# Performance work log

Hardware: AMD Instinct MI355X
Metric: run time of the kernel (lower is better)

## Reference

```python
import jax, jax.numpy as jnp
import numpy as np

B, T, D, H, W = 2, 16, 64, 64, 64
MAX_GROWTH = 0.0  # max_growth_rate init kwarg

def _ln(x, g, b):
    m = x.mean(-1, keepdims=True)
    v = x.var(-1, keepdims=True)
    return (x - m) * jax.lax.rsqrt(v + 1e-5) * g + b

def _pscan(A, X):
    # linear recurrence h_t = A_t*h_{t-1} + X_t via Blelchlo-style associative scan over axis 1
    def comb(l, r):
        a1, x1 = l
        a2, x2 = r
        return a1 * a2, a2 * x1 + x2
    return jax.lax.associative_scan(comb, (A, X), axis=1)[1]

def setup_inputs() -> dict:
    key = jax.random.key(0)
    ks = jax.random.split(key, 20)
    n = lambda k, s, sc=1.0: jax.random.normal(k, s, dtype=jnp.float32) * sc
    inp = dict(
        x_re=n(ks[0], (B, T, D, H, W)), x_im=n(ks[1], (B, T, D, H, W)),
        h_re=n(ks[2], (B * H * W, 1, D)), h_im=n(ks[3], (B * H * W, 1, D)),
        flux_re=n(ks[4], (B, D)), flux_im=n(ks[5], (B, D)),
        dt_seq=0.01 + 0.1 * jax.random.uniform(ks[6], (B, T), dtype=jnp.float32),
        g_s=jnp.ones(2 * D, jnp.float32), b_s=jnp.zeros(2 * D, jnp.float32),
        Wc=n(ks[7], (3, 3, 2 * D, 2 * D), 1.0 / np.sqrt(9 * 2 * D)), bc=jnp.zeros(2 * D, jnp.float32),
        g_t=jnp.ones(2 * D, jnp.float32), b_t=jnp.zeros(2 * D, jnp.float32),
        E_re=n(ks[8], (D, D), 1.0 / np.sqrt(D)), E_im=n(ks[9], (D, D), 1.0 / np.sqrt(D)),
        Dec_re=n(ks[10], (D, D), 1.0 / np.sqrt(D)), Dec_im=n(ks[11], (D, D), 1.0 / np.sqrt(D)),
        lam_flux_raw=jnp.zeros(D, jnp.float32),
        Wsrc_re=n(ks[12], (D, D), 1.0 / np.sqrt(D)), Wsrc_im=n(ks[13], (D, D), 1.0 / np.sqrt(D)),
        w_gate=n(ks[14], (D,)), b_gate=jnp.zeros(D, jnp.float32),
        lam_re_raw=jnp.ones(D, jnp.float32), lam_im=n(ks[15], (D,)),
        W1=n(ks[16], (2 * D, 8 * D), 1.0 / np.sqrt(2 * D)), b1=jnp.zeros(8 * D, jnp.float32),
        W2=n(ks[17], (8 * D, 2 * D), 1.0 / np.sqrt(8 * D)), b2=jnp.zeros(2 * D, jnp.float32),
    )
    return inp

def _forward(x_re, x_im, h_re, h_im, flux_re, flux_im, dt_seq, g_s, b_s, Wc, bc, g_t, b_t,
             E_re, E_im, Dec_re, Dec_im, lam_flux_raw, Wsrc_re, Wsrc_im, w_gate, b_gate,
             lam_re_raw, lam_im, W1, b1, W2, b2):
    # channel-last complex field (B,T,H,W,D)
    x = jnp.moveaxis(x_re, 2, -1) + 1j * jnp.moveaxis(x_im, 2, -1)
    # --- spatial residual branch: LN -> Clifford(= real 2D conv on [re;im] channels) ---
    xr = jnp.concatenate([x.real, x.imag], -1)  # (B,T,H,W,2D)
    xn = _ln(xr, g_s, b_s).reshape(B * T, H, W, 2 * D)
    xs = jax.lax.conv_general_dilated(xn, Wc, (1, 1), 'SAME',
                                      dimension_numbers=('NHWC', 'HWIO', 'NHWC')) + bc
    xs = xs.reshape(B, T, H, W, 2 * D)
    x = x + (xs[..., :D] + 1j * xs[..., D:])
    # --- eigen-basis encode ---
    x_eig = jnp.einsum('bthwd,de->bthwe', x, E_re + 1j * E_im)
    x_mean = x_eig.mean((2, 3))  # (B,T,D)
    # --- flux tracker scan ---
    lam_f = jax.nn.softplus(lam_flux_raw)
    A_flux = jnp.exp(-lam_f * dt_seq[..., None])  # (B,T,D) real decay
    flux = _pscan(A_flux.astype(x_mean.dtype), x_mean * dt_seq[..., None])
    flux = flux + (flux_re + 1j * flux_im)[:, None, :] * jnp.cumprod(A_flux, axis=1)
    source = jnp.einsum('btd,de->bte', flux, Wsrc_re + 1j * Wsrc_im)
    gate = jax.nn.sigmoid(flux.real * w_gate + b_gate)  # real gate in [0,1]
    flux_out = flux[:, -1]
    ge = gate[:, :, None, None, :]
    forcing = x_eig * ge + source[:, :, None, None, :] * (1.0 - ge)
    # --- temporal propagator (exact exponential integrator) ---
    lam = (MAX_GROWTH - jax.nn.softplus(lam_re_raw)) + 1j * lam_im  # Re(lam) <= max_growth_rate
    op_decay = jnp.exp(lam * dt_seq[..., None])            # (B,T,D)
    op_forcing = (op_decay - 1.0) / lam
    u = forcing * op_forcing[:, :, None, None, :]          # (B,T,H,W,D)
    h_prev = (h_re + 1j * h_im).reshape(B, H, W, D)
    u = u.at[:, 0].add(h_prev * op_decay[:, 0][:, None, None, :])
    A_full = jnp.broadcast_to(op_decay[:, :, None, None, :], u.shape)
    u_out = _pscan(A_full, u)                              # (B,T,H,W,D)
    h_out = u_out[:, -1].reshape(B * H * W, 1, D)
    # --- decode + temporal LN/FFN residual ---
    decoded = jnp.einsum('bthwd,de->bthwe', u_out, Dec_re + 1j * Dec_im)
    dn = _ln(jnp.concatenate([decoded.real, decoded.imag], -1), g_t, b_t)
    h1 = jax.nn.gelu(jnp.einsum('bthwc,cf->bthwf', dn, W1) + b1)
    d2 = jnp.einsum('bthwf,fc->bthwc', h1, W2) + b2
    delta = d2[..., :D] + 1j * d2[..., D:]
    z = x + decoded + delta
    return z, h_out, flux_out

def reference(x_re, x_im, h_re, h_im, flux_re, flux_im, dt_seq, g_s, b_s, Wc, bc, g_t, b_t,
              E_re, E_im, Dec_re, Dec_im, lam_flux_raw, Wsrc_re, Wsrc_im, w_gate, b_gate,
              lam_re_raw, lam_im, W1, b1, W2, b2):
    z, h_out, flux_out = _forward(x_re, x_im, h_re, h_im, flux_re, flux_im, dt_seq, g_s, b_s,
                                  Wc, bc, g_t, b_t, E_re, E_im, Dec_re, Dec_im, lam_flux_raw,
                                  Wsrc_re, Wsrc_im, w_gate, b_gate, lam_re_raw, lam_im,
                                  W1, b1, W2, b2)
    # complex outputs returned as real/imag stacked on last axis
    return (jnp.stack([z.real, z.imag], -1),
            jnp.stack([h_out.real, h_out.imag], -1),
            jnp.stack([flux_out.real, flux_out.imag], -1))
```

## Files before the change

### kernel.cpp

```cpp
#include <hip/hip_runtime.h>
#include <hip/hip_bf16.h>


typedef __hip_bfloat16 bf16;
typedef __attribute__((ext_vector_type(8))) short bhalf8;
typedef __attribute__((ext_vector_type(4))) float floatx4;

#define DEV __device__ __forceinline__

DEV float b2f(const bf16 x) { return __bfloat162float(x); }
DEV bf16  f2b(float x)      { return __float2bfloat16(x); }
DEV unsigned short f2bu(float x) { bf16 h = f2b(x); return *(unsigned short*)&h; }
DEV float bu2f(unsigned short u) { unsigned int t = ((unsigned int)u) << 16; return *(float*)&t; }
DEV float softplusf(float x){ return x > 20.f ? x : log1pf(expf(x)); }
DEV float geluf(float x) {
    float v = x * fmaf(x * x, 0.10294324f, 2.30220819f);
    float e = __builtin_amdgcn_exp2f(-v);
    return x * __builtin_amdgcn_rcpf(1.f + e);
}

static constexpr int B_ = 2, T_ = 16, D_ = 64, HW = 4096;
static constexpr int NPIX = B_ * T_ * HW;
static constexpr long long N1 = (long long)NPIX * 128;

static constexpr long long BUFA  = 0;
static constexpr long long XUBF  = N1;
static constexpr long long DECBF = N1 + N1 / 2;
static constexpr long long XNBF  = 2 * N1;
static constexpr long long XCBF  = 2 * N1 + N1 / 2;
static constexpr long long XMEAN = 3 * N1;
static constexpr long long TABS  = XMEAN + 4096;
static constexpr long long FLAGO = TABS + 14336;
static constexpr long long WCP   = FLAGO + 64;
static constexpr long long W1P   = WCP + 73728;
static constexpr long long W2P   = W1P + 32768;
static constexpr long long WEP   = W2P + 32768;
static constexpr long long WDP   = WEP + 8192;

static constexpr long long ZOUT = 0;
static constexpr long long HOUT = 16777216;
static constexpr long long FOUT = 17825792;

DEV float ld(const void* p, long long i, bool bf) {
    if (bf) return b2f(((const bf16*)p)[i]);
    return ((const float*)p)[i];
}

__global__ void k_detect(const unsigned short* __restrict__ x, float* __restrict__ ws) {
    int lane = threadIdx.x;
    int cnt = 0;
    for (int i = lane; i < 256; i += 64) {
        int e = (x[i] >> 7) & 0xFF;
        cnt += (e >= 100 && e <= 140) ? 1 : 0;
    }
    for (int m = 1; m < 64; m <<= 1) cnt += __shfl_xor(cnt, m, 64);
    if (lane == 0) ws[FLAGO] = (cnt >= 224) ? 1.f : 0.f;
}

__global__ void k_convert(const void* Wc, const void* W1, const void* W2,
                          const void* Er, const void* Ei, const void* Dr, const void* Di,
                          float* ws) {
    bool bf = ws[FLAGO] != 0.f;
    int i = blockIdx.x * 256 + threadIdx.x;
    unsigned short* wcp = (unsigned short*)(ws + WCP);
    unsigned short* w1p = (unsigned short*)(ws + W1P);
    unsigned short* w2p = (unsigned short*)(ws + W2P);
    unsigned short* wep = (unsigned short*)(ws + WEP);
    unsigned short* wdp = (unsigned short*)(ws + WDP);
    if (i < 147456) {
        int j = i & 7, lane = (i >> 3) & 63, nt = (i >> 9) & 7, kc = (i >> 12) & 3, tap = i >> 14;
        int ic = kc * 32 + ((lane >> 4) << 3) + j, oc = nt * 16 + (lane & 15);
        wcp[i] = f2bu(ld(Wc, tap * 16384 + ic * 128 + oc, bf)); return;
    } i -= 147456;
    if (i < 65536) {
        int j = i & 7, lane = (i >> 3) & 63, nt = (i >> 9) & 31, kc = i >> 14;
        int ic = kc * 32 + ((lane >> 4) << 3) + j, oc = nt * 16 + (lane & 15);
        w1p[i] = f2bu(ld(W1, ic * 512 + oc, bf)); return;
    } i -= 65536;
    if (i < 65536) {
        int j = i & 7, lane = (i >> 3) & 63, nt = (i >> 9) & 7, kc = i >> 12;
        int ic = kc * 32 + ((lane >> 4) << 3) + j, oc = nt * 16 + (lane & 15);
        w2p[i] = f2bu(ld(W2, ic * 128 + oc, bf)); return;
    } i -= 65536;
    if (i < 16384) {
        int j = i & 7, lane = (i >> 3) & 63, nt = (i >> 9) & 7, kc = i >> 12;
        int k = kc * 32 + ((lane >> 4) << 3) + j, n = nt * 16 + (lane & 15);
        float v;
        if (k < 64) v = (n < 64) ? ld(Er, k * 64 + n, bf) : ld(Ei, k * 64 + (n - 64), bf);
        else        v = (n < 64) ? -ld(Ei, (k - 64) * 64 + n, bf) : ld(Er, (k - 64) * 64 + (n - 64), bf);
        wep[i] = f2bu(v); return;
    } i -= 16384;
    if (i < 16384) {
        int j = i & 7, lane = (i >> 3) & 63, nt = (i >> 9) & 7, kc = i >> 12;
        int k = kc * 32 + ((lane >> 4) << 3) + j, n = nt * 16 + (lane & 15);
        float v;
        if (k < 64) v = (n < 64) ? ld(Dr, k * 64 + n, bf) : ld(Di, k * 64 + (n - 64), bf);
        else        v = (n < 64) ? -ld(Di, (k - 64) * 64 + n, bf) : ld(Dr, (k - 64) * 64 + (n - 64), bf);
        wdp[i] = f2bu(v); return;
    }
}

__global__ __launch_bounds__(256) void kA_ln(const void* __restrict__ xre,
                                             const void* __restrict__ xim,
                                             const void* __restrict__ gs,
                                             const void* __restrict__ bs,
                                             float* __restrict__ ws) {
    __shared__ unsigned short sr[64][72] __attribute__((aligned(16)));
    __shared__ unsigned short si[64][72] __attribute__((aligned(16)));
    __shared__ float red[2][4][64];
    __shared__ float mv[64], rv[64], gb[256];
    bool bf = ws[FLAGO] != 0.f;
    int blk = blockIdx.x;
    int bt = blk >> 6;
    int px0 = (blk & 63) * 64;
    int tid = threadIdx.x;
    gb[tid] = (tid < 128) ? ld(gs, tid, bf) : ld(bs, tid - 128, bf);
    if (bf) {
        const unsigned short* xr16 = (const unsigned short*)xre;
        const unsigned short* xi16 = (const unsigned short*)xim;
        for (int l = tid; l < 1024; l += 256) {
            int a = l >> 9, dd = (l >> 3) & 63, ck = l & 7;
            long long src = (long long)bt * 262144 + (long long)dd * 4096 + px0 + ck * 8;
            bhalf8 v = *(const bhalf8*)&(a ? xi16 : xr16)[src];
            *(bhalf8*)&(a ? si : sr)[dd][ck * 8] = v;
        }
    } else {
        for (int l = tid; l < 8192; l += 256) {
            int a = l >> 12, dd = (l >> 6) & 63, px = l & 63;
            float v = ((const float*)(a ? xim : xre))[(long long)bt * 262144 + (long long)dd * 4096 + px0 + px];
            (a ? si : sr)[dd][px] = f2bu(v);
        }
    }
    __syncthreads();
    int px = tid & 63, part = tid >> 6;
    float s = 0.f, ss = 0.f;
    for (int d = part * 16; d < part * 16 + 16; d++) {
        float r = bu2f(sr[d][px]), q = bu2f(si[d][px]);
        s += r + q; ss += r * r + q * q;
    }
    red[0][part][px] = s; red[1][part][px] = ss;
    __syncthreads();
    if (tid < 64) {
        float S  = red[0][0][tid] + red[0][1][tid] + red[0][2][tid] + red[0][3][tid];
        float SS = red[1][0][tid] + red[1][1][tid] + red[1][2][tid] + red[1][3][tid];
        float m = S * (1.f / 128.f);
        mv[tid] = m;
        rv[tid] = rsqrtf(SS * (1.f / 128.f) - m * m + 1e-5f);
    }
    __syncthreads();
    unsigned short* xcb = (unsigned short*)(ws + XCBF);
    unsigned short* xnb = (unsigned short*)(ws + XNBF);
    long long pbase = ((long long)bt * 4096 + px0) * 128;
    for (int l = tid; l < 8192; l += 256) {
        int p2 = l >> 7, ch = l & 127, d = ch & 63;
        unsigned short raw = (ch < 64 ? sr : si)[d][p2];
        float v = bu2f(raw);
        xcb[pbase + p2 * 128 + ch] = raw;
        xnb[pbase + p2 * 128 + ch] = f2bu((v - mv[p2]) * rv[p2] * gb[ch] + gb[128 + ch]);
    }
}

__global__ __launch_bounds__(256) void kB_conv(const void* __restrict__ bc,
                                               float* __restrict__ ws) {
    __shared__ unsigned short xt[3][64][136] __attribute__((aligned(16)));
    bool bf = ws[FLAGO] != 0.f;
    int blk = blockIdx.x, bt = blk >> 6, h = blk & 63;
    int tid = threadIdx.x, lane = tid & 63, wv = tid >> 6;
    int m16 = lane & 15, quad = lane >> 4;
    const unsigned short* xnb = (const unsigned short*)(ws + XNBF);
    const unsigned short* wcp = (const unsigned short*)(ws + WCP);
    bhalf8 zero8 = {0, 0, 0, 0, 0, 0, 0, 0};
    for (int l = tid; l < 3072; l += 256) {
        int r = l >> 10, rem = l & 1023, col = rem >> 4, ck = rem & 15;
        int hr = h - 1 + r;
        bhalf8 v = zero8;
        if (hr >= 0 && hr < 64)
            v = *(const bhalf8*)&xnb[(((long long)bt * 4096 + hr * 64 + col) << 7) + ck * 8];
        *(bhalf8*)&xt[r][col][ck * 8] = v;
    }
    __syncthreads();
    floatx4 acc[4][2];
    #pragma unroll
    for (int mt = 0; mt < 4; mt++)
        #pragma unroll
        for (int nt = 0; nt < 2; nt++)
            acc[mt][nt] = (floatx4){0.f, 0.f, 0.f, 0.f};
    for (int tap = 0; tap < 9; tap++) {
        int dy = tap / 3, dx = tap - dy * 3;
        #pragma unroll
        for (int kc = 0; kc < 4; kc++) {
            bhalf8 bfr[2];
            #pragma unroll
            for (int nt = 0; nt < 2; nt++)
                bfr[nt] = *(const bhalf8*)&wcp[((((tap * 4 + kc) * 8) + (wv * 2 + nt)) * 64 + lane) * 8];
            #pragma unroll
            for (int mt = 0; mt < 4; mt++) {
                int col = mt * 16 + m16 + dx - 1;
                bhalf8 af = zero8;
                if (col >= 0 && col < 64)
                    af = *(const bhalf8*)&xt[dy][col][kc * 32 + quad * 8];
                acc[mt][0] = __builtin_amdgcn_mfma_f32_16x16x32_bf16(af, bfr[0], acc[mt][0], 0, 0, 0);
                acc[mt][1] = __builtin_amdgcn_mfma_f32_16x16x32_bf16(af, bfr[1], acc[mt][1], 0, 0, 0);
            }
        }
    }
    __syncthreads();
    unsigned short (*At)[136] = (unsigned short(*)[136])&xt[0][0][0];
    const unsigned short* xcb = (const unsigned short*)(ws + XCBF);
    unsigned short* xub = (unsigned short*)(ws + XUBF);
    #pragma unroll
    for (int nt = 0; nt < 2; nt++) {
        int n = wv * 32 + nt * 16 + m16;
        float bcv = ld(bc, n, bf);
        #pragma unroll
        for (int mt = 0; mt < 4; mt++)
            #pragma unroll
            for (int r = 0; r < 4; r++) {
                int m = mt * 16 + quad * 4 + r;
                long long p = (long long)bt * 4096 + h * 64 + m;
                unsigned short u = f2bu(acc[mt][nt][r] + bu2f(xcb[p * 128 + n]) + bcv);
                xub[p * 128 + n] = u;
                At[m][n] = u;
            }
    }
    __syncthreads();
    const unsigned short* wep = (const unsigned short*)(ws + WEP);
    long long px0 = (long long)blk * 64;
    floatx4 acce[4][2];
    #pragma unroll
    for (int mt = 0; mt < 4; mt++)
        #pragma unroll
        for (int nt = 0; nt < 2; nt++)
            acce[mt][nt] = (floatx4){0.f, 0.f, 0.f, 0.f};
    #pragma unroll
    for (int kc = 0; kc < 4; kc++) {
        bhalf8 bfr[2];
        #pragma unroll
        for (int nt = 0; nt < 2; nt++)
            bfr[nt] = *(const bhalf8*)&wep[(((kc * 8) + wv * 2 + nt) * 64 + lane) * 8];
        #pragma unroll
        for (int mt = 0; mt < 4; mt++) {
            bhalf8 af = *(const bhalf8*)&At[mt * 16 + m16][kc * 32 + quad * 8];
            acce[mt][0] = __builtin_amdgcn_mfma_f32_16x16x32_bf16(af, bfr[0], acce[mt][0], 0, 0, 0);
            acce[mt][1] = __builtin_amdgcn_mfma_f32_16x16x32_bf16(af, bfr[1], acce[mt][1], 0, 0, 0);
        }
    }
    unsigned short* xeb = (unsigned short*)(ws + BUFA);
    #pragma unroll
    for (int nt = 0; nt < 2; nt++) {
        int n = wv * 32 + nt * 16 + m16;
        float part = 0.f;
        #pragma unroll
        for (int mt = 0; mt < 4; mt++)
            #pragma unroll
            for (int r = 0; r < 4; r++) {
                int m = mt * 16 + quad * 4 + r;
                xeb[(px0 + m) * 128 + n] = f2bu(acce[mt][nt][r]);
                part += acce[mt][nt][r];
            }
        part += __shfl_xor(part, 16, 64);
        part += __shfl_xor(part, 32, 64);
        if (quad == 0) atomicAdd(ws + XMEAN + bt * 128 + n, part);
    }
}

__global__ __launch_bounds__(256) void kD_flux(const void* __restrict__ fxr, const void* __restrict__ fxi,
                                               const void* __restrict__ dtseq, const void* __restrict__ lamflux,
                                               const void* __restrict__ Wsr, const void* __restrict__ Wsi,
                                               const void* __restrict__ wgate, const void* __restrict__ bgate,
                                               const void* __restrict__ lamreraw, const void* __restrict__ lamim,
                                               float* __restrict__ ws, void* __restrict__ outv) {
    bool bfo = ws[FLAGO] != 0.f;
    int b = blockIdx.x;
    int tid = threadIdx.x;
    int d = tid & 63, g = tid >> 6;
    __shared__ float fr[64], fi[64], psr[4][64], psi[4][64];
    float lam_f = softplusf(ld(lamflux, d, bfo));
    float lre = -softplusf(ld(lamreraw, d, bfo));
    float lim = ld(lamim, d, bfo);
    float cr = 0.f, ci = 0.f;
    if (g == 0) { cr = ld(fxr, b * 64 + d, bfo); ci = ld(fxi, b * 64 + d, bfo); }
    float* tabs = ws + TABS;
    const float* xmean = ws + XMEAN;
    for (int t = 0; t < 16; t++) {
        float dt = ld(dtseq, b * 16 + t, bfo);
        int idx = b * 1024 + t * 64 + d;
        if (g == 0) {
            float A = expf(-lam_f * dt);
            float xr = xmean[(b * 16 + t) * 128 + d]      * (1.f / 4096.f) * dt;
            float xq = xmean[(b * 16 + t) * 128 + 64 + d] * (1.f / 4096.f) * dt;
            cr = A * cr + xr; ci = A * ci + xq;
            fr[d] = cr; fi[d] = ci;
        }
        __syncthreads();
        {
            float pr = 0.f, pi = 0.f;
            #pragma unroll
            for (int k = 0; k < 16; k++) {
                int d2 = g * 16 + k;
                float wr = ld(Wsr, d2 * 64 + d, bfo), wi = ld(Wsi, d2 * 64 + d, bfo);
                pr += fr[d2] * wr - fi[d2] * wi;
                pi += fr[d2] * wi + fi[d2] * wr;
            }
            psr[g][d] = pr; psi[g][d] = pi;
        }
        if (g == 1) {
            float od  = expf(lre * dt);
            float odr = od * cosf(lim * dt);
            float odi = od * sinf(lim * dt);
            tabs[3 * 2048 + idx] = odr; tabs[4 * 2048 + idx] = odi;
            float den = lre * lre + lim * lim;
            float tr = odr - 1.f;
            tabs[5 * 2048 + idx] = (tr * lre + odi * lim) / den;
            tabs[6 * 2048 + idx] = (odi * lre - tr * lim) / den;
        }
        __syncthreads();
        if (g == 0) {
            float sr = psr[0][d] + psr[1][d] + psr[2][d] + psr[3][d];
            float si2 = psi[0][d] + psi[1][d] + psi[2][d] + psi[3][d];
            tabs[1 * 2048 + idx] = sr; tabs[2 * 2048 + idx] = si2;
            tabs[0 * 2048 + idx] = 1.f / (1.f + expf(-(cr * ld(wgate, d, bfo) + ld(bgate, d, bfo))));
            if (t == 15) {
                if (bfo) {
                    bf16* ob = (bf16*)outv;
                    ob[FOUT + (b * 64 + d) * 2]     = f2b(cr);
                    ob[FOUT + (b * 64 + d) * 2 + 1] = f2b(ci);
                } else {
                    float* of = (float*)outv;
                    of[FOUT + (b * 64 + d) * 2]     = cr;
                    of[FOUT + (b * 64 + d) * 2 + 1] = ci;
                }
            }
        }
    }
}

__global__ __launch_bounds__(256) void kE_scan(const void* __restrict__ hre,
                                               const void* __restrict__ him,
                                               float* __restrict__ ws, void* __restrict__ outv) {
    __shared__ float tab[7][16][64];
    bool bfo = ws[FLAGO] != 0.f;
    int tid = threadIdx.x;
    long long G = (long long)blockIdx.x * 256 + tid;
    int d0 = (int)(G & 31) * 2;
    int pixg = (int)(G >> 5);
    int pix = pixg & 4095;
    int b = pixg >> 12;
    const float* tabs = ws + TABS;
    for (int l = tid; l < 7 * 1024; l += 256) {
        int a = l >> 10, idx = l & 1023;
        ((float*)tab)[l] = tabs[a * 2048 + b * 1024 + idx];
    }
    __syncthreads();
    long long hidx = ((long long)b * 4096 + pix) * 64 + d0;
    float cr0, ci0, cr1, ci1;
    if (bfo) {
        unsigned int r2 = *(const unsigned int*)&((const unsigned short*)hre)[hidx];
        unsigned int i2 = *(const unsigned int*)&((const unsigned short*)him)[hidx];
        cr0 = bu2f((unsigned short)(r2 & 0xffff)); cr1 = bu2f((unsigned short)(r2 >> 16));
        ci0 = bu2f((unsigned short)(i2 & 0xffff)); ci1 = bu2f((unsigned short)(i2 >> 16));
    } else {
        float2 r2 = *(const float2*)((const float*)hre + hidx);
        float2 i2 = *(const float2*)((const float*)him + hidx);
        cr0 = r2.x; cr1 = r2.y; ci0 = i2.x; ci1 = i2.y;
    }
    const unsigned short* xe = (const unsigned short*)(ws + BUFA);
    unsigned short* ub = (unsigned short*)(ws + XCBF);
    for (int t = 0; t < 16; t++) {
        long long base = ((long long)((b * 16 + t) * 4096 + pix)) * 128 + d0;
        unsigned int xr2 = *(const unsigned int*)&xe[base];
        unsigned int xi2 = *(const unsigned int*)&xe[base + 64];
        float2 gt2  = *(const float2*)&tab[0][t][d0];
        float2 sr2  = *(const float2*)&tab[1][t][d0];
        float2 si2  = *(const float2*)&tab[2][t][d0];
        float2 odr2 = *(const float2*)&tab[3][t][d0];
        float2 odi2 = *(const float2*)&tab[4][t][d0];
        float2 ofr2 = *(const float2*)&tab[5][t][d0];
        float2 ofi2 = *(const float2*)&tab[6][t][d0];
        {
            float xr = bu2f((unsigned short)(xr2 & 0xffff));
            float xi = bu2f((unsigned short)(xi2 & 0xffff));
            float fre = xr * gt2.x + sr2.x * (1.f - gt2.x);
            float fim = xi * gt2.x + si2.x * (1.f - gt2.x);
            float ure = fre * ofr2.x - fim * ofi2.x;
            float uim = fre * ofi2.x + fim * ofr2.x;
            float n0 = odr2.x * cr0 - odi2.x * ci0 + ure;
            float n1 = odr2.x * ci0 + odi2.x * cr0 + uim;
            cr0 = n0; ci0 = n1;
        }
        {
            float xr = bu2f((unsigned short)(xr2 >> 16));
            float xi = bu2f((unsigned short)(xi2 >> 16));
            float fre = xr * gt2.y + sr2.y * (1.f - gt2.y);
            float fim = xi * gt2.y + si2.y * (1.f - gt2.y);
            float ure = fre * ofr2.y - fim * ofi2.y;
            float uim = fre * ofi2.y + fim * ofr2.y;
            float n0 = odr2.y * cr1 - odi2.y * ci1 + ure;
            float n1 = odr2.y * ci1 + odi2.y * cr1 + uim;
            cr1 = n0; ci1 = n1;
        }
        *(unsigned int*)&ub[base]      = (unsigned int)f2bu(cr0) | ((unsigned int)f2bu(cr1) << 16);
        *(unsigned int*)&ub[base + 64] = (unsigned int)f2bu(ci0) | ((unsigned int)f2bu(ci1) << 16);
    }
    if (bfo) {
        uint2 hv;
        hv.x = (unsigned int)f2bu(cr0) | ((unsigned int)f2bu(ci0) << 16);
        hv.y = (unsigned int)f2bu(cr1) | ((unsigned int)f2bu(ci1) << 16);
        *(uint2*)((unsigned short*)outv + HOUT + 2 * hidx) = hv;
    } else {
        float4 hv; hv.x = cr0; hv.y = ci0; hv.z = cr1; hv.w = ci1;
        *(float4*)((float*)outv + HOUT + 2 * hidx) = hv;
    }
}

__global__ __launch_bounds__(256, 4) void kMLP(const void* __restrict__ gt_,
                                               const void* __restrict__ bt_,
                                               const void* __restrict__ b1v,
                                               const void* __restrict__ b2v,
                                               float* __restrict__ ws, void* __restrict__ outv) {
    __shared__ unsigned char POOL[16384] __attribute__((aligned(16)));
    __shared__ unsigned short Dt[32][136] __attribute__((aligned(16)));
    __shared__ unsigned short A1[32][136] __attribute__((aligned(16)));
    __shared__ float gbt[256];
    __shared__ float gb2[128];
    __shared__ float psS[4][32], psQ[4][32];
    __shared__ float mvv[32], rvv[32];
    unsigned short (*UA)[136] = (unsigned short(*)[136])POOL;
    unsigned short (*h1f)[2][64][8] = (unsigned short(*)[2][64][8])POOL;
    bool bf = ws[FLAGO] != 0.f;
    long long px0 = (long long)blockIdx.x * 32;
    int tid = threadIdx.x, lane = tid & 63, wv = tid >> 6;
    int m16 = lane & 15, quad = lane >> 4;
    gbt[tid] = (tid < 128) ? ld(gt_, tid, bf) : ld(bt_, tid - 128, bf);
    if (tid < 128) gb2[tid] = ld(b2v, tid, bf);
    const unsigned short* uo = (const unsigned short*)(ws + XCBF);
    for (int l = tid; l < 512; l += 256) {
        int p2 = l >> 4, ck = l & 15;
        *(bhalf8*)&UA[p2][ck * 8] = *(const bhalf8*)&uo[(px0 + p2) * 128 + ck * 8];
    }
    __syncthreads();
    const unsigned short* wdp = (const unsigned short*)(ws + WDP);
    floatx4 accd[2][2];
    #pragma unroll
    for (int mt = 0; mt < 2; mt++)
        #pragma unroll
        for (int nt = 0; nt < 2; nt++)
            accd[mt][nt] = (floatx4){0.f, 0.f, 0.f, 0.f};
    #pragma unroll
    for (int kc = 0; kc < 4; kc++) {
        bhalf8 bfr0 = *(const bhalf8*)&wdp[(((kc * 8) + wv * 2 + 0) * 64 + lane) * 8];
        bhalf8 bfr1 = *(const bhalf8*)&wdp[(((kc * 8) + wv * 2 + 1) * 64 + lane) * 8];
        bhalf8 af0 = *(const bhalf8*)&UA[m16][kc * 32 + quad * 8];
        bhalf8 af1 = *(const bhalf8*)&UA[16 + m16][kc * 32 + quad * 8];
        accd[0][0] = __builtin_amdgcn_mfma_f32_16x16x32_bf16(af0, bfr0, accd[0][0], 0, 0, 0);
        accd[0][1] = __builtin_amdgcn_mfma_f32_16x16x32_bf16(af0, bfr1, accd[0][1], 0, 0, 0);
        accd[1][0] = __builtin_amdgcn_mfma_f32_16x16x32_bf16(af1, bfr0, accd[1][0], 0, 0, 0);
        accd[1][1] = __builtin_amdgcn_mfma_f32_16x16x32_bf16(af1, bfr1, accd[1][1], 0, 0, 0);
    }
    #pragma unroll
    for (int mt = 0; mt < 2; mt++)
        #pragma unroll
        for (int r = 0; r < 4; r++) {
            int mrow = mt * 16 + quad * 4 + r;
            float a0 = accd[mt][0][r], a1 = accd[mt][1][r];
            Dt[mrow][wv * 32 + m16]      = f2bu(a0);
            Dt[mrow][wv * 32 + 16 + m16] = f2bu(a1);
            float s = a0 + a1, q = a0 * a0 + a1 * a1;
            #pragma unroll
            for (int msk = 1; msk <= 8; msk <<= 1) {
                s += __shfl_xor(s, msk, 64);
                q += __shfl_xor(q, msk, 64);
            }
            if (m16 == 0) { psS[wv][mrow] = s; psQ[wv][mrow] = q; }
        }
    __syncthreads();
    if (tid < 32) {
        float S = psS[0][tid] + psS[1][tid] + psS[2][tid] + psS[3][tid];
        float Q = psQ[0][tid] + psQ[1][tid] + psQ[2][tid] + psQ[3][tid];
        float m = S * (1.f / 128.f);
        mvv[tid] = m;
        rvv[tid] = rsqrtf(Q * (1.f / 128.f) - m * m + 1e-5f);
    }
    __syncthreads();
    #pragma unroll
    for (int mt = 0; mt < 2; mt++)
        #pragma unroll
        for (int r = 0; r < 4; r++) {
            int mrow = mt * 16 + quad * 4 + r;
            float mu = mvv[mrow], rs = rvv[mrow];
            #pragma unroll
            for (int nt = 0; nt < 2; nt++) {
                int n = wv * 32 + nt * 16 + m16;
                A1[mrow][n] = f2bu((accd[mt][nt][r] - mu) * rs * gbt[n] + gbt[128 + n]);
            }
        }
    __syncthreads();
    const unsigned short* w1p = (const unsigned short*)(ws + W1P);
    const unsigned short* w2p = (const unsigned short*)(ws + W2P);
    floatx4 acc2[2][2];
    #pragma unroll
    for (int mt = 0; mt < 2; mt++)
        #pragma unroll
        for (int nt = 0; nt < 2; nt++)
            acc2[mt][nt] = (floatx4){0.f, 0.f, 0.f, 0.f};
    #pragma unroll
    for (int ph = 0; ph < 2; ph++) {
        floatx4 acc1[2][4];
        #pragma unroll
        for (int mt = 0; mt < 2; mt++)
            #pragma unroll
            for (int nt4 = 0; nt4 < 4; nt4++)
                acc1[mt][nt4] = (floatx4){0.f, 0.f, 0.f, 0.f};
        #pragma unroll
        for (int kc = 0; kc < 4; kc++) {
            bhalf8 af0 = *(const bhalf8*)&A1[m16][kc * 32 + quad * 8];
            bhalf8 af1 = *(const bhalf8*)&A1[16 + m16][kc * 32 + quad * 8];
            #pragma unroll
            for (int nt4 = 0; nt4 < 4; nt4++) {
                int nt = ph * 4 + nt4;
                bhalf8 bfr = *(const bhalf8*)&w1p[(((kc * 32) + wv * 8 + nt) * 64 + lane) * 8];
                acc1[0][nt4] = __builtin_amdgcn_mfma_f32_16x16x32_bf16(af0, bfr, acc1[0][nt4], 0, 0, 0);
                acc1[1][nt4] = __builtin_amdgcn_mfma_f32_16x16x32_bf16(af1, bfr, acc1[1][nt4], 0, 0, 0);
            }
        }
        if (ph == 0) __syncthreads();
        #pragma unroll
        for (int nt4 = 0; nt4 < 4; nt4++) {
            int nt = ph * 4 + nt4;
            int n = (wv * 8 + nt) * 16 + m16;
            float b1f = ld(b1v, n, bf);
            int qp = ((nt * 2) + (m16 >> 3)) & 3;
            int slot = wv * 2 + (nt4 >> 1);
            int j = m16 & 7;
            #pragma unroll
            for (int mt = 0; mt < 2; mt++)
                #pragma unroll
                for (int r = 0; r < 4; r++)
                    h1f[slot][mt][qp * 16 + quad * 4 + r][j] =
                        f2bu(geluf(acc1[mt][nt4][r] + b1f));
        }
        __syncthreads();
        #pragma unroll
        for (int s = 0; s < 8; s++) {
            int kc2g = (s >> 1) * 4 + (s & 1) + ph * 2;
            bhalf8 a0 = *(const bhalf8*)&h1f[s][0][lane][0];
            bhalf8 a1 = *(const bhalf8*)&h1f[s][1][lane][0];
            #pragma unroll
            for (int nt = 0; nt < 2; nt++) {
                bhalf8 bfr = *(const bhalf8*)&w2p[(((kc2g * 8) + wv * 2 + nt) * 64 + lane) * 8];
                acc2[0][nt] = __builtin_amdgcn_mfma_f32_16x16x32_bf16(a0, bfr, acc2[0][nt], 0, 0, 0);
                acc2[1][nt] = __builtin_amdgcn_mfma_f32_16x16x32_bf16(a1, bfr, acc2[1][nt], 0, 0, 0);
            }
        }
        if (ph == 0) __syncthreads();
    }
    #pragma unroll
    for (int nt = 0; nt < 2; nt++) {
        int n = wv * 32 + nt * 16 + m16;
        #pragma unroll
        for (int mt = 0; mt < 2; mt++)
            #pragma unroll
            for (int r = 0; r < 4; r++)
                A1[mt * 16 + quad * 4 + r][n] = f2bu(acc2[mt][nt][r]);
    }
    __syncthreads();
    {
        const unsigned short* xub = (const unsigned short*)(ws + XUBF);
        int pxl = tid >> 3, dc = (tid & 7) * 8;
        long long p = px0 + pxl;
        bhalf8 cre = *(const bhalf8*)&A1[pxl][dc];
        bhalf8 cim = *(const bhalf8*)&A1[pxl][64 + dc];
        bhalf8 xr8 = *(const bhalf8*)&xub[p * 128 + dc];
        bhalf8 xi8 = *(const bhalf8*)&xub[p * 128 + 64 + dc];
        bhalf8 dr8 = *(const bhalf8*)&Dt[pxl][dc];
        bhalf8 di8 = *(const bhalf8*)&Dt[pxl][64 + dc];
        float zr[8], zi[8];
        #pragma unroll
        for (int k = 0; k < 8; k++) {
            zr[k] = bu2f((unsigned short)cre[k]) + gb2[dc + k]
                  + bu2f((unsigned short)xr8[k]) + bu2f((unsigned short)dr8[k]);
            zi[k] = bu2f((unsigned short)cim[k]) + gb2[64 + dc + k]
                  + bu2f((unsigned short)xi8[k]) + bu2f((unsigned short)di8[k]);
        }
        if (bf) {
            unsigned short o[16];
            #pragma unroll
            for (int k = 0; k < 8; k++) { o[2 * k] = f2bu(zr[k]); o[2 * k + 1] = f2bu(zi[k]); }
            unsigned short* ob = (unsigned short*)outv;
            *(bhalf8*)&ob[ZOUT + p * 128 + 2 * dc]     = *(bhalf8*)&o[0];
            *(bhalf8*)&ob[ZOUT + p * 128 + 2 * dc + 8] = *(bhalf8*)&o[8];
        } else {
            float* of = (float*)outv + ZOUT + p * 128 + 2 * dc;
            #pragma unroll
            for (int k = 0; k < 8; k++) { of[2 * k] = zr[k]; of[2 * k + 1] = zi[k]; }
        }
    }
}

extern "C" void kernel_launch(void* const* d_in, const int* in_sizes, int n_in,
                              void* d_out, int out_size, void* d_ws, size_t ws_size,
                              hipStream_t stream) {
    const void* x_re  = d_in[0];
    const void* x_im  = d_in[1];
    const void* h_re  = d_in[2];
    const void* h_im  = d_in[3];
    const void* fl_re = d_in[4];
    const void* fl_im = d_in[5];
    const void* dtseq = d_in[6];
    const void* g_s   = d_in[7];
    const void* b_s   = d_in[8];
    const void* Wc    = d_in[9];
    const void* bc    = d_in[10];
    const void* g_t   = d_in[11];
    const void* b_t   = d_in[12];
    const void* E_re  = d_in[13];
    const void* E_im  = d_in[14];
    const void* De_re = d_in[15];
    const void* De_im = d_in[16];
    const void* lamfl = d_in[17];
    const void* Ws_re = d_in[18];
    const void* Ws_im = d_in[19];
    const void* wgate = d_in[20];
    const void* bgate = d_in[21];
    const void* lamrr = d_in[22];
    const void* lamim = d_in[23];
    const void* W1    = d_in[24];
    const void* b1    = d_in[25];
    const void* W2    = d_in[26];
    const void* b2    = d_in[27];
    float* ws = (float*)d_ws;

    hipMemsetAsync((char*)d_ws + XMEAN * sizeof(float), 0, 4096 * sizeof(float), stream);
    k_detect<<<1, 64, 0, stream>>>((const unsigned short*)x_re, ws);
    k_convert<<<1216, 256, 0, stream>>>(Wc, W1, W2, E_re, E_im, De_re, De_im, ws);
    kA_ln<<<2048, 256, 0, stream>>>(x_re, x_im, g_s, b_s, ws);
    kB_conv<<<2048, 256, 0, stream>>>(bc, ws);
    kD_flux<<<2, 256, 0, stream>>>(fl_re, fl_im, dtseq, lamfl, Ws_re, Ws_im,
                                   wgate, bgate, lamrr, lamim, ws, d_out);
    kE_scan<<<1024, 256, 0, stream>>>(h_re, h_im, ws, d_out);
    kMLP<<<4096, 256, 0, stream>>>(g_t, b_t, b1, b2, ws, d_out);
}
```

Before: 414.9 us.

## Double MLP kernel pixel tile to 64 rows and keep decoded residual in registers

The fused decode/LN/FFN kernel now processes 64 pixels per block instead of 32, so each weight fragment loaded from the workspace feeds four MFMA row tiles instead of two. The grid is halved and launch bounds are lowered to two blocks per CU to make room for the larger register and LDS footprint. The decoded tile is no longer staged in shared memory as bf16. It is added to the FFN output from the accumulator registers before the final store, which also drops one rounding step. The trade is fewer resident waves and higher register pressure in exchange for less weight-load traffic per pixel.

```diff
diff --git a/kernel.cpp b/kernel.cpp
--- a/kernel.cpp
+++ b/kernel.cpp
@@ -413,36 +413,35 @@
     }
 }
 
-__global__ __launch_bounds__(256, 4) void kMLP(const void* __restrict__ gt_,
+__global__ __launch_bounds__(256, 2) void kMLP(const void* __restrict__ gt_,
                                                const void* __restrict__ bt_,
                                                const void* __restrict__ b1v,
                                                const void* __restrict__ b2v,
                                                float* __restrict__ ws, void* __restrict__ outv) {
-    __shared__ unsigned char POOL[16384] __attribute__((aligned(16)));
-    __shared__ unsigned short Dt[32][136] __attribute__((aligned(16)));
-    __shared__ unsigned short A1[32][136] __attribute__((aligned(16)));
+    __shared__ unsigned char POOL[32768] __attribute__((aligned(16)));
+    __shared__ unsigned short A1[64][136] __attribute__((aligned(16)));
     __shared__ float gbt[256];
     __shared__ float gb2[128];
-    __shared__ float psS[4][32], psQ[4][32];
-    __shared__ float mvv[32], rvv[32];
+    __shared__ float psS[4][64], psQ[4][64];
+    __shared__ float mvv[64], rvv[64];
     unsigned short (*UA)[136] = (unsigned short(*)[136])POOL;
-    unsigned short (*h1f)[2][64][8] = (unsigned short(*)[2][64][8])POOL;
+    unsigned short (*h1f)[4][64][8] = (unsigned short(*)[4][64][8])POOL;
     bool bf = ws[FLAGO] != 0.f;
-    long long px0 = (long long)blockIdx.x * 32;
+    long long px0 = (long long)blockIdx.x * 64;
     int tid = threadIdx.x, lane = tid & 63, wv = tid >> 6;
     int m16 = lane & 15, quad = lane >> 4;
     gbt[tid] = (tid < 128) ? ld(gt_, tid, bf) : ld(bt_, tid - 128, bf);
     if (tid < 128) gb2[tid] = ld(b2v, tid, bf);
     const unsigned short* uo = (const unsigned short*)(ws + XCBF);
-    for (int l = tid; l < 512; l += 256) {
+    for (int l = tid; l < 1024; l += 256) {
         int p2 = l >> 4, ck = l & 15;
         *(bhalf8*)&UA[p2][ck * 8] = *(const bhalf8*)&uo[(px0 + p2) * 128 + ck * 8];
     }
     __syncthreads();
     const unsigned short* wdp = (const unsigned short*)(ws + WDP);
-    floatx4 accd[2][2];
-    #pragma unroll
-    for (int mt = 0; mt < 2; mt++)
+    floatx4 accd[4][2];
+    #pragma unroll
+    for (int mt = 0; mt < 4; mt++)
         #pragma unroll
         for (int nt = 0; nt < 2; nt++)
             accd[mt][nt] = (floatx4){0.f, 0.f, 0.f, 0.f};
@@ -450,21 +449,19 @@
     for (int kc = 0; kc < 4; kc++) {
         bhalf8 bfr0 = *(const bhalf8*)&wdp[(((kc * 8) + wv * 2 + 0) * 64 + lane) * 8];
         bhalf8 bfr1 = *(const bhalf8*)&wdp[(((kc * 8) + wv * 2 + 1) * 64 + lane) * 8];
-        bhalf8 af0 = *(const bhalf8*)&UA[m16][kc * 32 + quad * 8];
-        bhalf8 af1 = *(const bhalf8*)&UA[16 + m16][kc * 32 + quad * 8];
-        accd[0][0] = __builtin_amdgcn_mfma_f32_16x16x32_bf16(af0, bfr0, accd[0][0], 0, 0, 0);
-        accd[0][1] = __builtin_amdgcn_mfma_f32_16x16x32_bf16(af0, bfr1, accd[0][1], 0, 0, 0);
-        accd[1][0] = __builtin_amdgcn_mfma_f32_16x16x32_bf16(af1, bfr0, accd[1][0], 0, 0, 0);
-        accd[1][1] = __builtin_amdgcn_mfma_f32_16x16x32_bf16(af1, bfr1, accd[1][1], 0, 0, 0);
-    }
-    #pragma unroll
-    for (int mt = 0; mt < 2; mt++)
+        #pragma unroll
+        for (int mt = 0; mt < 4; mt++) {
+            bhalf8 af = *(const bhalf8*)&UA[mt * 16 + m16][kc * 32 + quad * 8];
+            accd[mt][0] = __builtin_amdgcn_mfma_f32_16x16x32_bf16(af, bfr0, accd[mt][0], 0, 0, 0);
+            accd[mt][1] = __builtin_amdgcn_mfma_f32_16x16x32_bf16(af, bfr1, accd[mt][1], 0, 0, 0);
+        }
+    }
+    #pragma unroll
+    for (int mt = 0; mt < 4; mt++)
         #pragma unroll
         for (int r = 0; r < 4; r++) {
             int mrow = mt * 16 + quad * 4 + r;
             float a0 = accd[mt][0][r], a1 = accd[mt][1][r];
-            Dt[mrow][wv * 32 + m16]      = f2bu(a0);
-            Dt[mrow][wv * 32 + 16 + m16] = f2bu(a1);
             float s = a0 + a1, q = a0 * a0 + a1 * a1;
             #pragma unroll
             for (int msk = 1; msk <= 8; msk <<= 1) {
@@ -474,7 +471,7 @@
             if (m16 == 0) { psS[wv][mrow] = s; psQ[wv][mrow] = q; }
         }
     __syncthreads();
-    if (tid < 32) {
+    if (tid < 64) {
         float S = psS[0][tid] + psS[1][tid] + psS[2][tid] + psS[3][tid];
         float Q = psQ[0][tid] + psQ[1][tid] + psQ[2][tid] + psQ[3][tid];
         float m = S * (1.f / 128.f);
@@ -483,7 +480,7 @@
     }
     __syncthreads();
     #pragma unroll
-    for (int mt = 0; mt < 2; mt++)
+    for (int mt = 0; mt < 4; mt++)
         #pragma unroll
         for (int r = 0; r < 4; r++) {
             int mrow = mt * 16 + quad * 4 + r;
@@ -497,33 +494,35 @@
     __syncthreads();
     const unsigned short* w1p = (const unsigned short*)(ws + W1P);
     const unsigned short* w2p = (const unsigned short*)(ws + W2P);
-    floatx4 acc2[2][2];
-    #pragma unroll
-    for (int mt = 0; mt < 2; mt++)
+    floatx4 acc2[4][2];
+    #pragma unroll
+    for (int mt = 0; mt < 4; mt++)
         #pragma unroll
         for (int nt = 0; nt < 2; nt++)
             acc2[mt][nt] = (floatx4){0.f, 0.f, 0.f, 0.f};
     #pragma unroll
     for (int ph = 0; ph < 2; ph++) {
-        floatx4 acc1[2][4];
-        #pragma unroll
-        for (int mt = 0; mt < 2; mt++)
+        floatx4 acc1[4][4];
+        #pragma unroll
+        for (int mt = 0; mt < 4; mt++)
             #pragma unroll
             for (int nt4 = 0; nt4 < 4; nt4++)
                 acc1[mt][nt4] = (floatx4){0.f, 0.f, 0.f, 0.f};
         #pragma unroll
         for (int kc = 0; kc < 4; kc++) {
-            bhalf8 af0 = *(const bhalf8*)&A1[m16][kc * 32 + quad * 8];
-            bhalf8 af1 = *(const bhalf8*)&A1[16 + m16][kc * 32 + quad * 8];
+            bhalf8 af[4];
+            #pragma unroll
+            for (int mt = 0; mt < 4; mt++)
+                af[mt] = *(const bhalf8*)&A1[mt * 16 + m16][kc * 32 + quad * 8];
             #pragma unroll
             for (int nt4 = 0; nt4 < 4; nt4++) {
                 int nt = ph * 4 + nt4;
                 bhalf8 bfr = *(const bhalf8*)&w1p[(((kc * 32) + wv * 8 + nt) * 64 + lane) * 8];
-                acc1[0][nt4] = __builtin_amdgcn_mfma_f32_16x16x32_bf16(af0, bfr, acc1[0][nt4], 0, 0, 0);
-                acc1[1][nt4] = __builtin_amdgcn_mfma_f32_16x16x32_bf16(af1, bfr, acc1[1][nt4], 0, 0, 0);
-            }
-        }
-        if (ph == 0) __syncthreads();
+                #pragma unroll
+                for (int mt = 0; mt < 4; mt++)
+                    acc1[mt][nt4] = __builtin_amdgcn_mfma_f32_16x16x32_bf16(af[mt], bfr, acc1[mt][nt4], 0, 0, 0);
+            }
+        }
         #pragma unroll
         for (int nt4 = 0; nt4 < 4; nt4++) {
             int nt = ph * 4 + nt4;
@@ -533,7 +532,7 @@
             int slot = wv * 2 + (nt4 >> 1);
             int j = m16 & 7;
             #pragma unroll
-            for (int mt = 0; mt < 2; mt++)
+            for (int mt = 0; mt < 4; mt++)
                 #pragma unroll
                 for (int r = 0; r < 4; r++)
                     h1f[slot][mt][qp * 16 + quad * 4 + r][j] =
@@ -543,13 +542,16 @@
         #pragma unroll
         for (int s = 0; s < 8; s++) {
             int kc2g = (s >> 1) * 4 + (s & 1) + ph * 2;
-            bhalf8 a0 = *(const bhalf8*)&h1f[s][0][lane][0];
-            bhalf8 a1 = *(const bhalf8*)&h1f[s][1][lane][0];
+            bhalf8 a[4];
+            #pragma unroll
+            for (int mt = 0; mt < 4; mt++)
+                a[mt] = *(const bhalf8*)&h1f[s][mt][lane][0];
             #pragma unroll
             for (int nt = 0; nt < 2; nt++) {
                 bhalf8 bfr = *(const bhalf8*)&w2p[(((kc2g * 8) + wv * 2 + nt) * 64 + lane) * 8];
-                acc2[0][nt] = __builtin_amdgcn_mfma_f32_16x16x32_bf16(a0, bfr, acc2[0][nt], 0, 0, 0);
-                acc2[1][nt] = __builtin_amdgcn_mfma_f32_16x16x32_bf16(a1, bfr, acc2[1][nt], 0, 0, 0);
+                #pragma unroll
+                for (int mt = 0; mt < 4; mt++)
+                    acc2[mt][nt] = __builtin_amdgcn_mfma_f32_16x16x32_bf16(a[mt], bfr, acc2[mt][nt], 0, 0, 0);
             }
         }
         if (ph == 0) __syncthreads();
@@ -558,41 +560,39 @@
     for (int nt = 0; nt < 2; nt++) {
         int n = wv * 32 + nt * 16 + m16;
         #pragma unroll
-        for (int mt = 0; mt < 2; mt++)
+        for (int mt = 0; mt < 4; mt++)
             #pragma unroll
             for (int r = 0; r < 4; r++)
-                A1[mt * 16 + quad * 4 + r][n] = f2bu(acc2[mt][nt][r]);
+                A1[mt * 16 + quad * 4 + r][n] = f2bu(acc2[mt][nt][r] + accd[mt][nt][r]);
     }
     __syncthreads();
     {
         const unsigned short* xub = (const unsigned short*)(ws + XUBF);
-        int pxl = tid >> 3, dc = (tid & 7) * 8;
-        long long p = px0 + pxl;
-        bhalf8 cre = *(const bhalf8*)&A1[pxl][dc];
-        bhalf8 cim = *(const bhalf8*)&A1[pxl][64 + dc];
-        bhalf8 xr8 = *(const bhalf8*)&xub[p * 128 + dc];
-        bhalf8 xi8 = *(const bhalf8*)&xub[p * 128 + 64 + dc];
-        bhalf8 dr8 = *(const bhalf8*)&Dt[pxl][dc];
-        bhalf8 di8 = *(const bhalf8*)&Dt[pxl][64 + dc];
-        float zr[8], zi[8];
-        #pragma unroll
-        for (int k = 0; k < 8; k++) {
-            zr[k] = bu2f((unsigned short)cre[k]) + gb2[dc + k]
-                  + bu2f((unsigned short)xr8[k]) + bu2f((unsigned short)dr8[k]);
-            zi[k] = bu2f((unsigned short)cim[k]) + gb2[64 + dc + k]
-                  + bu2f((unsigned short)xi8[k]) + bu2f((unsigned short)di8[k]);
-        }
-        if (bf) {
-            unsigned short o[16];
-            #pragma unroll
-            for (int k = 0; k < 8; k++) { o[2 * k] = f2bu(zr[k]); o[2 * k + 1] = f2bu(zi[k]); }
-            unsigned short* ob = (unsigned short*)outv;
-            *(bhalf8*)&ob[ZOUT + p * 128 + 2 * dc]     = *(bhalf8*)&o[0];
-            *(bhalf8*)&ob[ZOUT + p * 128 + 2 * dc + 8] = *(bhalf8*)&o[8];
-        } else {
-            float* of = (float*)outv + ZOUT + p * 128 + 2 * dc;
-            #pragma unroll
-            for (int k = 0; k < 8; k++) { of[2 * k] = zr[k]; of[2 * k + 1] = zi[k]; }
+        for (int l = tid; l < 512; l += 256) {
+            int row = l >> 3, dc = (l & 7) * 8;
+            long long p = px0 + row;
+            bhalf8 cre = *(const bhalf8*)&A1[row][dc];
+            bhalf8 cim = *(const bhalf8*)&A1[row][64 + dc];
+            bhalf8 xr8 = *(const bhalf8*)&xub[p * 128 + dc];
+            bhalf8 xi8 = *(const bhalf8*)&xub[p * 128 + 64 + dc];
+            float zr[8], zi[8];
+            #pragma unroll
+            for (int k = 0; k < 8; k++) {
+                zr[k] = bu2f((unsigned short)cre[k]) + gb2[dc + k] + bu2f((unsigned short)xr8[k]);
+                zi[k] = bu2f((unsigned short)cim[k]) + gb2[64 + dc + k] + bu2f((unsigned short)xi8[k]);
+            }
+            if (bf) {
+                unsigned short o[16];
+                #pragma unroll
+                for (int k = 0; k < 8; k++) { o[2 * k] = f2bu(zr[k]); o[2 * k + 1] = f2bu(zi[k]); }
+                unsigned short* ob = (unsigned short*)outv;
+                *(bhalf8*)&ob[ZOUT + p * 128 + 2 * dc]     = *(bhalf8*)&o[0];
+                *(bhalf8*)&ob[ZOUT + p * 128 + 2 * dc + 8] = *(bhalf8*)&o[8];
+            } else {
+                float* of = (float*)outv + ZOUT + p * 128 + 2 * dc;
+                #pragma unroll
+                for (int k = 0; k < 8; k++) { of[2 * k] = zr[k]; of[2 * k + 1] = zi[k]; }
+            }
         }
     }
 }
@@ -638,5 +638,5 @@
     kD_flux<<<2, 256, 0, stream>>>(fl_re, fl_im, dtseq, lamfl, Ws_re, Ws_im,
                                    wgate, bgate, lamrr, lamim, ws, d_out);
     kE_scan<<<1024, 256, 0, stream>>>(h_re, h_im, ws, d_out);
-    kMLP<<<4096, 256, 0, stream>>>(g_t, b_t, b1, b2, ws, d_out);
-}
+    kMLP<<<2048, 256, 0, stream>>>(g_t, b_t, b1, b2, ws, d_out);
+}
```

New measurement: 457.9 us. 10.4% more time.
